# Optimization experiments

Measured on AMD Instinct MI355X. Metric: run time of the kernel, lower is better.

The kernel has to match this reference:

```python
import jax, jax.numpy as jnp
import numpy as np
import math

N_HEAD = 12


def setup_inputs() -> dict:
    key = jax.random.key(0)
    ks = jax.random.split(key, 4)
    B, T, C = 8, 1024, 768
    s = 0.02
    return {
        "x": jax.random.normal(ks[0], (B, T, C), dtype=jnp.float32),
        "attn_mask": jnp.ones((B, T), dtype=jnp.int32),
        "W_attn": jax.random.normal(ks[1], (C, 3 * C), dtype=jnp.float32) * s,
        "b_attn": jnp.zeros((3 * C,), dtype=jnp.float32),
        "W_proj": jax.random.normal(ks[2], (C, C), dtype=jnp.float32) * s,
        "b_proj": jnp.zeros((C,), dtype=jnp.float32),
    }


def reference(x, attn_mask, W_attn, b_attn, W_proj, b_proj):
    B, T, C = x.shape
    hd = C // N_HEAD
    qkv = x @ W_attn + b_attn                      # [B, T, 3C]
    q, k, v = jnp.split(qkv, 3, axis=2)
    # [B, H, T, hd]
    q = q.reshape(B, T, N_HEAD, hd).transpose(0, 2, 1, 3)
    k = k.reshape(B, T, N_HEAD, hd).transpose(0, 2, 1, 3)
    v = v.reshape(B, T, N_HEAD, hd).transpose(0, 2, 1, 3)
    scores = jnp.einsum("bhqd,bhkd->bhqk", q, k) * (1.0 / math.sqrt(hd))
    mask = attn_mask[:, None, None, :]             # [B, 1, 1, T] broadcast over H, q
    scores = jnp.where(mask == 0, -jnp.inf, scores)
    attn = jax.nn.softmax(scores, axis=-1)
    out = jnp.einsum("bhqk,bhkd->bhqd", attn, v)   # [B, H, T, hd]
    out = out.transpose(0, 2, 1, 3).reshape(B, T, C)
    return out @ W_proj + b_proj
```

## Files before the change

### kernel.cpp

```cpp
#include <hip/hip_runtime.h>
#include <hip/hip_bf16.h>
#include <math.h>

constexpr int Bsz  = 8;
constexpr int Tseq = 1024;
constexpr int Cdim = 768;
constexpr int NH   = 12;
constexpr int HD   = 64;
constexpr int Mrows = Bsz * Tseq;
constexpr int C3    = 3 * Cdim;

using short8  = __attribute__((ext_vector_type(8))) short;
using s4v     = __attribute__((ext_vector_type(4))) short;
using floatx4 = __attribute__((ext_vector_type(4))) float;
using uintx4  = __attribute__((ext_vector_type(4))) unsigned int;

__device__ __forceinline__ unsigned short f32_to_bf16_rn(float f) {
    unsigned int u = __float_as_uint(f);
    unsigned int r = u + 0x7FFFu + ((u >> 16) & 1u);
    return (unsigned short)(r >> 16);
}
__device__ __forceinline__ unsigned pack_bf16x2_rn(float a, float b) {
    float2 f2; f2.x = a; f2.y = b;
    __hip_bfloat162 h = __float22bfloat162_rn(f2);
    unsigned r;
    __builtin_memcpy(&r, &h, sizeof(r));
    return r;
}
__device__ __forceinline__ short8 lds_ld8(const unsigned short* p) {
    s4v a = *(const s4v*)p;
    s4v b = *(const s4v*)(p + 4);
    return __builtin_shufflevector(a, b, 0, 1, 2, 3, 4, 5, 6, 7);
}
__device__ __forceinline__ void lds_st8(unsigned short* p, short8 v) {
    *(s4v*)p       = __builtin_shufflevector(v, v, 0, 1, 2, 3);
    *(s4v*)(p + 4) = __builtin_shufflevector(v, v, 4, 5, 6, 7);
}

#define GLOAD_LDS16(g, l) __builtin_amdgcn_global_load_lds(                    \
    (const __attribute__((address_space(1))) void*)(g),                        \
    (__attribute__((address_space(3))) void*)(l), 16, 0, 0)

#define WAITVM0 asm volatile("s_waitcnt vmcnt(0)" ::: "memory")

__global__ __launch_bounds__(256)
void to_bf16(const float* __restrict__ in, unsigned short* __restrict__ out, int n4)
{
    int t = blockIdx.x * blockDim.x + threadIdx.x;
    if (t >= n4) return;
    float4 v = ((const float4*)in)[t];
    ushort4 o;
    o.x = f32_to_bf16_rn(v.x);
    o.y = f32_to_bf16_rn(v.y);
    o.z = f32_to_bf16_rn(v.z);
    o.w = f32_to_bf16_rn(v.w);
    ((ushort4*)out)[t] = o;
}

__global__ __launch_bounds__(256)
void transpose_bf16(const float* __restrict__ in, unsigned short* __restrict__ out,
                    int K, int N)
{
    __shared__ float tile[32][33];
    const int k0 = blockIdx.y * 32, n0 = blockIdx.x * 32;
    const int tx = threadIdx.x & 31, ty = threadIdx.x >> 5;
    #pragma unroll
    for (int r = ty; r < 32; r += 8)
        tile[r][tx] = in[(size_t)(k0 + r) * N + n0 + tx];
    __syncthreads();
    #pragma unroll
    for (int r = ty; r < 32; r += 8)
        out[(size_t)(n0 + r) * K + k0 + tx] = f32_to_bf16_rn(tile[tx][r]);
}

template<bool HM, bool B16>
__device__ __forceinline__ void gemm_body_128x256(
    const unsigned short* __restrict__ A_g,
    const unsigned short* __restrict__ B_g,
    const float* __restrict__ bias,
    void* __restrict__ Cout,
    const int row0, const int col0, const int K, const int N,
    unsigned short* lds)
{
    constexpr int BK   = 32;
    constexpr int ABUF = 4096;
    constexpr int BUFS = 12288;

    const int tid  = threadIdx.x;
    const int wave = tid >> 6;
    const int lane = tid & 63;
    const int lm   = lane & 15;
    const int quad = lane >> 4;
    const int NI   = K / BK;
    const int sq8  = (quad ^ ((lm ^ (lm >> 2)) & 3)) * 8;
    const int sr   = tid >> 2;
    const int sq   = tid & 3;

    floatx4 acc[8][4] = {};

    auto stageA = [&](int buf, int k0) {
        #pragma unroll
        for (int s = 0; s < 2; ++s) {
            const int r  = s * 64 + sr;
            const int gc = ((sq ^ ((r ^ (r >> 2)) & 3)) << 3);
            if constexpr (HM) {
                const int head = k0 >> 6;
                const int off  = (k0 & 63) + gc;
                GLOAD_LDS16(A_g + (size_t)head * (Mrows * HD) +
                            (size_t)(row0 + r) * HD + off,
                            lds + buf * BUFS + r * 32 + sq * 8);
            } else {
                GLOAD_LDS16(A_g + (size_t)(row0 + r) * K + k0 + gc,
                            lds + buf * BUFS + r * 32 + sq * 8);
            }
        }
    };
    auto stageB = [&](int buf, int k0) {
        #pragma unroll
        for (int s = 0; s < 4; ++s) {
            const int r  = s * 64 + sr;
            const int gc = ((sq ^ ((r ^ (r >> 2)) & 3)) << 3);
            GLOAD_LDS16(B_g + (size_t)(col0 + r) * K + k0 + gc,
                        lds + buf * BUFS + ABUF + r * 32 + sq * 8);
        }
    };

    stageA(0, 0);  stageB(0, 0);
    stageA(1, BK); stageB(1, BK);
    asm volatile("s_waitcnt vmcnt(6)" ::: "memory");
    __builtin_amdgcn_s_barrier();

    short8 af[4], bf[4];
    int cur = 0;
    for (int kt = 0; kt < NI; ++kt) {
        const unsigned short* bufA = lds + cur * BUFS;
        const unsigned short* bufB = bufA + ABUF;
        const int  stg  = (cur + 2 >= 3) ? cur - 1 : cur + 2;
        const int  k2   = (kt + 2) * BK;
        const bool doSt = (kt + 2 < NI);

        #pragma unroll
        for (int i = 0; i < 4; ++i)
            af[i] = *(const short8*)(bufA + (i * 16 + lm) * 32 + sq8);
        #pragma unroll
        for (int j = 0; j < 4; ++j)
            bf[j] = *(const short8*)(bufB + (wave * 64 + j * 16 + lm) * 32 + sq8);
        if (doSt) stageA(stg, k2);
        __builtin_amdgcn_s_barrier();
        __builtin_amdgcn_s_setprio(1);
        #pragma unroll
        for (int i = 0; i < 4; ++i)
            #pragma unroll
            for (int j = 0; j < 4; ++j)
                acc[i][j] = __builtin_amdgcn_mfma_f32_16x16x32_bf16(af[i], bf[j], acc[i][j], 0, 0, 0);
        __builtin_amdgcn_s_setprio(0);
        __builtin_amdgcn_s_barrier();

        #pragma unroll
        for (int i = 0; i < 4; ++i)
            af[i] = *(const short8*)(bufA + ((4 + i) * 16 + lm) * 32 + sq8);
        if (doSt) stageB(stg, k2);
        __builtin_amdgcn_s_barrier();
        __builtin_amdgcn_s_setprio(1);
        #pragma unroll
        for (int i = 0; i < 4; ++i)
            #pragma unroll
            for (int j = 0; j < 4; ++j)
                acc[4 + i][j] = __builtin_amdgcn_mfma_f32_16x16x32_bf16(af[i], bf[j], acc[4 + i][j], 0, 0, 0);
        __builtin_amdgcn_s_setprio(0);
        if (kt == NI - 2) { WAITVM0; }
        else if (kt < NI - 2) {
            asm volatile("s_waitcnt vmcnt(6)" ::: "memory");
        }
        __builtin_amdgcn_s_barrier();

        cur = (cur == 2) ? 0 : cur + 1;
    }
    asm volatile("" ::: "memory");

    if constexpr (B16) {
        unsigned short* Cb   = (unsigned short*)Cout;
        unsigned short* wbuf = lds + (NI % 3) * BUFS + wave * 1088;
        float bvj[4];
        #pragma unroll
        for (int j = 0; j < 4; ++j) bvj[j] = bias[col0 + wave * 64 + j * 16 + lm];
        #pragma unroll
        for (int i = 0; i < 8; ++i) {
            #pragma unroll
            for (int j = 0; j < 4; ++j) {
                #pragma unroll
                for (int r = 0; r < 4; ++r)
                    wbuf[(quad * 4 + r) * 68 + j * 16 + lm] = f32_to_bf16_rn(acc[i][j][r] + bvj[j]);
            }
            asm volatile("s_waitcnt lgkmcnt(0)" ::: "memory");
            #pragma unroll
            for (int p = 0; p < 2; ++p) {
                const int lrow  = p * 8 + (lane >> 3);
                const int lcol8 = (lane & 7) * 8;
                short8 v = lds_ld8(&wbuf[lrow * 68 + lcol8]);
                *(short8*)(Cb + (size_t)(row0 + i * 16 + lrow) * N +
                           col0 + wave * 64 + lcol8) = v;
            }
            asm volatile("s_waitcnt lgkmcnt(0)" ::: "memory");
        }
    } else {
        float* C = (float*)Cout;
        #pragma unroll
        for (int j = 0; j < 4; ++j) {
            const int col = col0 + wave * 64 + j * 16 + lm;
            const float bv = bias[col];
            #pragma unroll
            for (int i = 0; i < 8; ++i) {
                const int rowb = row0 + i * 16 + quad * 4;
                #pragma unroll
                for (int r = 0; r < 4; ++r)
                    C[(size_t)(rowb + r) * N + col] = acc[i][j][r] + bv;
            }
        }
    }
}

__global__ __launch_bounds__(256, 2)
void gemm_qkv128(const unsigned short* __restrict__ A_g,
                 const unsigned short* __restrict__ B_g,
                 const float* __restrict__ bias,
                 unsigned short* __restrict__ Cb)
{
    __shared__ __align__(16) unsigned short lds[3 * 12288];
    const int bid = blockIdx.x;
    const int sid = (bid & 7) * 72 + (bid >> 3);
    const int by  = sid & 63;
    const int bx  = sid >> 6;
    gemm_body_128x256<false, true>(A_g, B_g, bias, Cb,
                                   by * 128, bx * 256, Cdim, C3, lds);
}

__global__ __launch_bounds__(256, 3)
void gemm_proj128sq(const unsigned short* __restrict__ AO_g,
                    const unsigned short* __restrict__ B_g,
                    const float* __restrict__ bias,
                    float* __restrict__ C)
{
    constexpr int BK   = 32;
    constexpr int K    = Cdim, N = Cdim;
    constexpr int ABUF = 4096;
    constexpr int BUFS = 8192;
    __shared__ __align__(16) unsigned short lds[3 * BUFS];

    const int tid  = threadIdx.x;
    const int wave = tid >> 6;
    const int lane = tid & 63;
    const int lm   = lane & 15;
    const int quad = lane >> 4;
    const int wy   = wave >> 1, wx = wave & 1;
    const int bid  = blockIdx.x;
    const int sid  = (bid & 7) * 48 + (bid >> 3);
    const int row0 = (sid & 63) * 128;
    const int col0 = (sid >> 6) * 128;
    const int NI   = K / BK;
    const int sq8  = (quad ^ ((lm ^ (lm >> 2)) & 3)) * 8;
    const int sr   = tid >> 2;
    const int sq   = tid & 3;

    floatx4 acc[4][4] = {};

    auto stageA = [&](int buf, int k0) {
        #pragma unroll
        for (int s = 0; s < 2; ++s) {
            const int r  = s * 64 + sr;
            const int gc = ((sq ^ ((r ^ (r >> 2)) & 3)) << 3);
            const int head = k0 >> 6;
            const int off  = (k0 & 63) + gc;
            GLOAD_LDS16(AO_g + (size_t)head * (Mrows * HD) +
                        (size_t)(row0 + r) * HD + off,
                        lds + buf * BUFS + r * 32 + sq * 8);
        }
    };
    auto stageB = [&](int buf, int k0) {
        #pragma unroll
        for (int s = 0; s < 2; ++s) {
            const int r  = s * 64 + sr;
            const int gc = ((sq ^ ((r ^ (r >> 2)) & 3)) << 3);
            GLOAD_LDS16(B_g + (size_t)(col0 + r) * K + k0 + gc,
                        lds + buf * BUFS + ABUF + r * 32 + sq * 8);
        }
    };

    stageA(0, 0);  stageB(0, 0);
    stageA(1, BK); stageB(1, BK);
    asm volatile("s_waitcnt vmcnt(4)" ::: "memory");
    __builtin_amdgcn_s_barrier();

    short8 af[4], bf[4];
    int cur = 0;
    for (int kt = 0; kt < NI; ++kt) {
        const unsigned short* bufA = lds + cur * BUFS;
        const unsigned short* bufB = bufA + ABUF;
        const int  stg  = (cur + 2 >= 3) ? cur - 1 : cur + 2;
        const int  k2   = (kt + 2) * BK;
        const bool doSt = (kt + 2 < NI);

        #pragma unroll
        for (int i = 0; i < 4; ++i)
            af[i] = *(const short8*)(bufA + (wy * 64 + i * 16 + lm) * 32 + sq8);
        #pragma unroll
        for (int j = 0; j < 2; ++j)
            bf[j] = *(const short8*)(bufB + (wx * 64 + j * 16 + lm) * 32 + sq8);
        if (doSt) stageA(stg, k2);
        __builtin_amdgcn_s_barrier();
        __builtin_amdgcn_s_setprio(1);
        #pragma unroll
        for (int i = 0; i < 4; ++i)
            #pragma unroll
            for (int j = 0; j < 2; ++j)
                acc[i][j] = __builtin_amdgcn_mfma_f32_16x16x32_bf16(af[i], bf[j], acc[i][j], 0, 0, 0);
        __builtin_amdgcn_s_setprio(0);
        __builtin_amdgcn_s_barrier();

        #pragma unroll
        for (int j = 2; j < 4; ++j)
            bf[j] = *(const short8*)(bufB + (wx * 64 + j * 16 + lm) * 32 + sq8);
        if (doSt) stageB(stg, k2);
        __builtin_amdgcn_s_barrier();
        __builtin_amdgcn_s_setprio(1);
        #pragma unroll
        for (int i = 0; i < 4; ++i)
            #pragma unroll
            for (int j = 2; j < 4; ++j)
                acc[i][j] = __builtin_amdgcn_mfma_f32_16x16x32_bf16(af[i], bf[j], acc[i][j], 0, 0, 0);
        __builtin_amdgcn_s_setprio(0);
        if (kt == NI - 2) { WAITVM0; }
        else if (kt < NI - 2) {
            asm volatile("s_waitcnt vmcnt(4)" ::: "memory");
        }
        __builtin_amdgcn_s_barrier();

        cur = (cur == 2) ? 0 : cur + 1;
    }
    asm volatile("" ::: "memory");

    #pragma unroll
    for (int j = 0; j < 4; ++j) {
        const int col = col0 + wx * 64 + j * 16 + lm;
        const float bv = bias[col];
        #pragma unroll
        for (int i = 0; i < 4; ++i) {
            const int rowb = row0 + wy * 64 + i * 16 + quad * 4;
            #pragma unroll
            for (int r = 0; r < 4; ++r)
                C[(size_t)(rowb + r) * N + col] = acc[i][j][r] + bv;
        }
    }
}

__global__ __launch_bounds__(256, 3)
void attn_bf16(const unsigned short* __restrict__ qkv,
               const int* __restrict__ mask,
               unsigned short* __restrict__ outh)
{
    constexpr int LDW = 68;
    constexpr int NT  = Tseq / 64;
    __shared__ __align__(16) unsigned short Kh[2][64 * LDW];
    __shared__ __align__(16) unsigned short Vh[2][64 * LDW];
    __shared__ float maskadd[2][64];
    __shared__ int   mflag[2];

    const int tid  = threadIdx.x;
    const int wave = tid >> 6;
    const int lane = tid & 63;
    const int lm   = lane & 15;
    const int quad = lane >> 4;
    const int idx  = blockIdx.x;
    const int bh   = idx % (Bsz * NH);
    const int qb   = idx / (Bsz * NH);
    const int b    = bh / NH;
    const int h    = bh % NH;
    const int q0   = qb * 128;
    const float scale = 0.125f;

    short8 qf[2][2];
    #pragma unroll
    for (int mt = 0; mt < 2; ++mt) {
        const size_t qrow = (size_t)(b * Tseq + q0 + wave * 32 + mt * 16 + lm) * C3 + h * HD;
        #pragma unroll
        for (int kf = 0; kf < 2; ++kf)
            qf[mt][kf] = *(const short8*)(qkv + qrow + kf * 32 + quad * 8);
    }

    const int tr0 = (tid & 31) * 2;
    const int sc  = (tid >> 5) * 8;
    const int ps0 = (tr0 & 0x27) | ((tr0 & 0x10) >> 1) | ((tr0 & 0x08) << 1);
    const int smi = (tid & 0x27) | ((tid & 0x10) >> 1) | ((tid & 0x08) << 1);

    short8 kh0, kh1, vh0, vh1;
    float  mreg = 0.f;

    {
        const size_t g0 = (size_t)(b * Tseq + tr0) * C3 + Cdim + h * HD + sc;
        kh0 = *(const short8*)(qkv + g0);
        kh1 = *(const short8*)(qkv + g0 + C3);
        vh0 = *(const short8*)(qkv + g0 + Cdim);
        vh1 = *(const short8*)(qkv + g0 + Cdim + C3);
        lds_st8(&Kh[0][ps0 * LDW + sc], kh0);
        lds_st8(&Kh[0][(ps0 + 1) * LDW + sc], kh1);
        #pragma unroll
        for (int i = 0; i < 8; ++i) {
            unsigned int pv = (unsigned int)(unsigned short)vh0[i] |
                              ((unsigned int)(unsigned short)vh1[i] << 16);
            *(unsigned int*)&Vh[0][(sc + i) * LDW + tr0] = pv;
        }
        if (tid < 64) {
            mreg = (mask[b * Tseq + tid] == 0) ? -1e30f : 0.0f;
            const int f = __all(mreg == 0.0f);
            maskadd[0][smi] = mreg;
            if (tid == 0) mflag[0] = f;
        }
    }
    __syncthreads();

    floatx4 O[2][4] = {};
    float lsum[2] = {0.f, 0.f};

    for (int kt = 0; kt < NT; ++kt) {
        const int cur = kt & 1;
        const int nxt = cur ^ 1;
        const unsigned short* Khc = Kh[cur];
        const unsigned short* Vhc = Vh[cur];

        if (kt + 1 < NT) {
            const size_t g0 = (size_t)(b * Tseq + (kt + 1) * 64 + tr0) * C3 + Cdim + h * HD + sc;
            kh0 = *(const short8*)(qkv + g0);
            kh1 = *(const short8*)(qkv + g0 + C3);
            vh0 = *(const short8*)(qkv + g0 + Cdim);
            vh1 = *(const short8*)(qkv + g0 + Cdim + C3);
            if (tid < 64) mreg = (mask[b * Tseq + (kt + 1) * 64 + tid] == 0) ? -1e30f : 0.0f;
        }

        floatx4 S[2][4] = {};
        #pragma unroll
        for (int kf = 0; kf < 2; ++kf) {
            short8 kh[4];
            #pragma unroll
            for (int nt = 0; nt < 4; ++nt)
                kh[nt] = lds_ld8(&Khc[(nt * 16 + lm) * LDW + kf * 32 + quad * 8]);
            #pragma unroll
            for (int mt = 0; mt < 2; ++mt)
                #pragma unroll
                for (int nt = 0; nt < 4; ++nt)
                    S[mt][nt] = __builtin_amdgcn_mfma_f32_16x16x32_bf16(kh[nt], qf[mt][kf], S[mt][nt], 0, 0, 0);
        }

        const int nomask = mflag[cur];

        unsigned X[2][8];
        if (nomask) {
            #pragma unroll
            for (int mt = 0; mt < 2; ++mt) {
                #pragma unroll
                for (int nt = 0; nt < 4; ++nt) {
                    float p0 = __expf(S[mt][nt][0] * scale);
                    float p1 = __expf(S[mt][nt][1] * scale);
                    float p2 = __expf(S[mt][nt][2] * scale);
                    float p3 = __expf(S[mt][nt][3] * scale);
                    lsum[mt] += p0; lsum[mt] += p1;
                    lsum[mt] += p2; lsum[mt] += p3;
                    X[mt][nt * 2 + 0] = pack_bf16x2_rn(p0, p1);
                    X[mt][nt * 2 + 1] = pack_bf16x2_rn(p2, p3);
                }
            }
        } else {
            float madd[4][4];
            #pragma unroll
            for (int nt = 0; nt < 4; ++nt)
                #pragma unroll
                for (int r = 0; r < 4; ++r)
                    madd[nt][r] = maskadd[cur][nt * 16 + quad * 4 + r];
            #pragma unroll
            for (int mt = 0; mt < 2; ++mt) {
                #pragma unroll
                for (int nt = 0; nt < 4; ++nt) {
                    float p0 = __expf(S[mt][nt][0] * scale + madd[nt][0]);
                    float p1 = __expf(S[mt][nt][1] * scale + madd[nt][1]);
                    float p2 = __expf(S[mt][nt][2] * scale + madd[nt][2]);
                    float p3 = __expf(S[mt][nt][3] * scale + madd[nt][3]);
                    lsum[mt] += p0; lsum[mt] += p1;
                    lsum[mt] += p2; lsum[mt] += p3;
                    X[mt][nt * 2 + 0] = pack_bf16x2_rn(p0, p1);
                    X[mt][nt * 2 + 1] = pack_bf16x2_rn(p2, p3);
                }
            }
        }

        const bool qodd = (quad & 1);
        short8 pf[2][2];
        #pragma unroll
        for (int mt = 0; mt < 2; ++mt) {
            #pragma unroll
            for (int pr = 0; pr < 4; ++pr) {
                const int a  = (pr & 1) | ((pr & 2) << 1);
                const int b2 = a + 2;
                unsigned t = qodd ? X[mt][a] : X[mt][b2];
                t = (unsigned)__shfl_xor((int)t, 16);
                X[mt][a]  = qodd ? t : X[mt][a];
                X[mt][b2] = qodd ? X[mt][b2] : t;
            }
            uintx4 u0 = {X[mt][0], X[mt][1], X[mt][2], X[mt][3]};
            uintx4 u1 = {X[mt][4], X[mt][5], X[mt][6], X[mt][7]};
            __builtin_memcpy(&pf[mt][0], &u0, 16);
            __builtin_memcpy(&pf[mt][1], &u1, 16);
        }

        #pragma unroll
        for (int kf = 0; kf < 2; ++kf) {
            #pragma unroll
            for (int dt = 0; dt < 4; ++dt) {
                short8 vh = lds_ld8(&Vhc[(dt * 16 + lm) * LDW + kf * 32 + quad * 8]);
                #pragma unroll
                for (int mt = 0; mt < 2; ++mt)
                    O[mt][dt] = __builtin_amdgcn_mfma_f32_16x16x32_bf16(vh, pf[mt][kf], O[mt][dt], 0, 0, 0);
            }
        }

        if (kt + 1 < NT) {
            lds_st8(&Kh[nxt][ps0 * LDW + sc], kh0);
            lds_st8(&Kh[nxt][(ps0 + 1) * LDW + sc], kh1);
            #pragma unroll
            for (int i = 0; i < 8; ++i) {
                unsigned int pv = (unsigned int)(unsigned short)vh0[i] |
                                  ((unsigned int)(unsigned short)vh1[i] << 16);
                *(unsigned int*)&Vh[nxt][(sc + i) * LDW + tr0] = pv;
            }
            if (tid < 64) {
                const int f = __all(mreg == 0.0f);
                maskadd[nxt][smi] = mreg;
                if (tid == 0) mflag[nxt] = f;
            }
        }
        __syncthreads();
    }

    #pragma unroll
    for (int mt = 0; mt < 2; ++mt) {
        lsum[mt] += __shfl_xor(lsum[mt], 16);
        lsum[mt] += __shfl_xor(lsum[mt], 32);
        const float inv_l = 1.0f / lsum[mt];
        const size_t row = (size_t)h * (Mrows * HD) +
                           (size_t)(b * Tseq + q0 + wave * 32 + mt * 16 + lm) * HD;
        #pragma unroll
        for (int dt = 0; dt < 4; ++dt) {
            ushort4 hv;
            unsigned short* hp = &hv.x;
            #pragma unroll
            for (int r = 0; r < 4; ++r)
                hp[r] = f32_to_bf16_rn(O[mt][dt][r] * inv_l);
            *(ushort4*)(outh + row + dt * 16 + quad * 4) = hv;
        }
    }
}

extern "C" void kernel_launch(void* const* d_in, const int* in_sizes, int n_in,
                              void* d_out, int out_size, void* d_ws, size_t ws_size,
                              hipStream_t stream)
{
    const float* x      = (const float*)d_in[0];
    const int*   mask   = (const int*)  d_in[1];
    const float* W_attn = (const float*)d_in[2];
    const float* b_attn = (const float*)d_in[3];
    const float* W_proj = (const float*)d_in[4];
    const float* b_proj = (const float*)d_in[5];
    float* out = (float*)d_out;

    unsigned short* xh    = (unsigned short*)d_ws;
    unsigned short* wat_h = xh    + (size_t)Mrows * Cdim;
    unsigned short* wpt_h = wat_h + (size_t)C3 * Cdim;
    unsigned short* qkvh  = wpt_h + (size_t)Cdim * Cdim;
    unsigned short* aoh   = xh;

    dim3 blk(256);

    to_bf16<<<dim3(Mrows * Cdim / 4 / 256), blk, 0, stream>>>(x, xh, Mrows * Cdim / 4);
    transpose_bf16<<<dim3(C3 / 32, Cdim / 32), blk, 0, stream>>>(W_attn, wat_h, Cdim, C3);
    transpose_bf16<<<dim3(Cdim / 32, Cdim / 32), blk, 0, stream>>>(W_proj, wpt_h, Cdim, Cdim);

    gemm_qkv128<<<dim3(576), blk, 0, stream>>>(xh, wat_h, b_attn, qkvh);

    attn_bf16<<<dim3((Tseq / 128) * Bsz * NH), blk, 0, stream>>>(qkvh, mask, aoh);

    gemm_proj128sq<<<dim3(384), blk, 0, stream>>>(aoh, wpt_h, b_proj, out);
}
```

Before: 205.0 us.

## Fuse prep kernels, drop intra-iteration GEMM barriers, split softmax sum accumulators

Merges the bf16 conversion of x and the two weight transposes into one launch keyed on block index. Removes three of the four s_barriers per k-iteration in both GEMM main loops, relying on the triple-buffer distance for safety. In attention, replaces per-iteration address recomputation with incremented pointers and splits the row-sum into two accumulators to shorten the dependency chain. Dropping the barriers risks LDS read/write races between waves.

```diff
diff --git a/kernel.cpp b/kernel.cpp
--- a/kernel.cpp
+++ b/kernel.cpp
@@ -44,25 +44,35 @@
 #define WAITVM0 asm volatile("s_waitcnt vmcnt(0)" ::: "memory")
 
 __global__ __launch_bounds__(256)
-void to_bf16(const float* __restrict__ in, unsigned short* __restrict__ out, int n4)
-{
-    int t = blockIdx.x * blockDim.x + threadIdx.x;
-    if (t >= n4) return;
-    float4 v = ((const float4*)in)[t];
-    ushort4 o;
-    o.x = f32_to_bf16_rn(v.x);
-    o.y = f32_to_bf16_rn(v.y);
-    o.z = f32_to_bf16_rn(v.z);
-    o.w = f32_to_bf16_rn(v.w);
-    ((ushort4*)out)[t] = o;
-}
-
-__global__ __launch_bounds__(256)
-void transpose_bf16(const float* __restrict__ in, unsigned short* __restrict__ out,
-                    int K, int N)
+void prep_all(const float* __restrict__ x,      unsigned short* __restrict__ xh,
+              const float* __restrict__ W_attn, unsigned short* __restrict__ wat_h,
+              const float* __restrict__ W_proj, unsigned short* __restrict__ wpt_h)
 {
     __shared__ float tile[32][33];
-    const int k0 = blockIdx.y * 32, n0 = blockIdx.x * 32;
+    const int bid = blockIdx.x;
+    if (bid < 6144) {
+        const int t = bid * 256 + threadIdx.x;
+        float4 v = ((const float4*)x)[t];
+        ushort4 o;
+        o.x = f32_to_bf16_rn(v.x);
+        o.y = f32_to_bf16_rn(v.y);
+        o.z = f32_to_bf16_rn(v.z);
+        o.w = f32_to_bf16_rn(v.w);
+        ((ushort4*)xh)[t] = o;
+        return;
+    }
+    const float* in; unsigned short* out; int N, bx, by;
+    if (bid < 6144 + 1728) {
+        const int r = bid - 6144;
+        in = W_attn; out = wat_h; N = C3;
+        bx = r % 72; by = r / 72;
+    } else {
+        const int r = bid - 7872;
+        in = W_proj; out = wpt_h; N = Cdim;
+        bx = r % 24; by = r / 24;
+    }
+    const int K  = Cdim;
+    const int k0 = by * 32, n0 = bx * 32;
     const int tx = threadIdx.x & 31, ty = threadIdx.x >> 5;
     #pragma unroll
     for (int r = ty; r < 32; r += 8)
@@ -146,7 +156,6 @@
         for (int j = 0; j < 4; ++j)
             bf[j] = *(const short8*)(bufB + (wave * 64 + j * 16 + lm) * 32 + sq8);
         if (doSt) stageA(stg, k2);
-        __builtin_amdgcn_s_barrier();
         __builtin_amdgcn_s_setprio(1);
         #pragma unroll
         for (int i = 0; i < 4; ++i)
@@ -154,13 +163,11 @@
             for (int j = 0; j < 4; ++j)
                 acc[i][j] = __builtin_amdgcn_mfma_f32_16x16x32_bf16(af[i], bf[j], acc[i][j], 0, 0, 0);
         __builtin_amdgcn_s_setprio(0);
-        __builtin_amdgcn_s_barrier();
 
         #pragma unroll
         for (int i = 0; i < 4; ++i)
             af[i] = *(const short8*)(bufA + ((4 + i) * 16 + lm) * 32 + sq8);
         if (doSt) stageB(stg, k2);
-        __builtin_amdgcn_s_barrier();
         __builtin_amdgcn_s_setprio(1);
         #pragma unroll
         for (int i = 0; i < 4; ++i)
@@ -168,6 +175,7 @@
             for (int j = 0; j < 4; ++j)
                 acc[4 + i][j] = __builtin_amdgcn_mfma_f32_16x16x32_bf16(af[i], bf[j], acc[4 + i][j], 0, 0, 0);
         __builtin_amdgcn_s_setprio(0);
+
         if (kt == NI - 2) { WAITVM0; }
         else if (kt < NI - 2) {
             asm volatile("s_waitcnt vmcnt(6)" ::: "memory");
@@ -307,7 +315,6 @@
         for (int j = 0; j < 2; ++j)
             bf[j] = *(const short8*)(bufB + (wx * 64 + j * 16 + lm) * 32 + sq8);
         if (doSt) stageA(stg, k2);
-        __builtin_amdgcn_s_barrier();
         __builtin_amdgcn_s_setprio(1);
         #pragma unroll
         for (int i = 0; i < 4; ++i)
@@ -315,13 +322,11 @@
             for (int j = 0; j < 2; ++j)
                 acc[i][j] = __builtin_amdgcn_mfma_f32_16x16x32_bf16(af[i], bf[j], acc[i][j], 0, 0, 0);
         __builtin_amdgcn_s_setprio(0);
-        __builtin_amdgcn_s_barrier();
 
         #pragma unroll
         for (int j = 2; j < 4; ++j)
             bf[j] = *(const short8*)(bufB + (wx * 64 + j * 16 + lm) * 32 + sq8);
         if (doSt) stageB(stg, k2);
-        __builtin_amdgcn_s_barrier();
         __builtin_amdgcn_s_setprio(1);
         #pragma unroll
         for (int i = 0; i < 4; ++i)
@@ -329,6 +334,7 @@
             for (int j = 2; j < 4; ++j)
                 acc[i][j] = __builtin_amdgcn_mfma_f32_16x16x32_bf16(af[i], bf[j], acc[i][j], 0, 0, 0);
         __builtin_amdgcn_s_setprio(0);
+
         if (kt == NI - 2) { WAITVM0; }
         else if (kt < NI - 2) {
             asm volatile("s_waitcnt vmcnt(4)" ::: "memory");
@@ -395,12 +401,14 @@
     short8 kh0, kh1, vh0, vh1;
     float  mreg = 0.f;
 
+    size_t gcur = (size_t)(b * Tseq + tr0) * C3 + Cdim + h * HD + sc;
+    int    mcur = b * Tseq + tid;
+
     {
-        const size_t g0 = (size_t)(b * Tseq + tr0) * C3 + Cdim + h * HD + sc;
-        kh0 = *(const short8*)(qkv + g0);
-        kh1 = *(const short8*)(qkv + g0 + C3);
-        vh0 = *(const short8*)(qkv + g0 + Cdim);
-        vh1 = *(const short8*)(qkv + g0 + Cdim + C3);
+        kh0 = *(const short8*)(qkv + gcur);
+        kh1 = *(const short8*)(qkv + gcur + C3);
+        vh0 = *(const short8*)(qkv + gcur + Cdim);
+        vh1 = *(const short8*)(qkv + gcur + Cdim + C3);
         lds_st8(&Kh[0][ps0 * LDW + sc], kh0);
         lds_st8(&Kh[0][(ps0 + 1) * LDW + sc], kh1);
         #pragma unroll
@@ -410,7 +418,7 @@
             *(unsigned int*)&Vh[0][(sc + i) * LDW + tr0] = pv;
         }
         if (tid < 64) {
-            mreg = (mask[b * Tseq + tid] == 0) ? -1e30f : 0.0f;
+            mreg = (mask[mcur] == 0) ? -1e30f : 0.0f;
             const int f = __all(mreg == 0.0f);
             maskadd[0][smi] = mreg;
             if (tid == 0) mflag[0] = f;
@@ -419,7 +427,8 @@
     __syncthreads();
 
     floatx4 O[2][4] = {};
-    float lsum[2] = {0.f, 0.f};
+    float lsA[2] = {0.f, 0.f};
+    float lsB[2] = {0.f, 0.f};
 
     for (int kt = 0; kt < NT; ++kt) {
         const int cur = kt & 1;
@@ -428,12 +437,13 @@
         const unsigned short* Vhc = Vh[cur];
 
         if (kt + 1 < NT) {
-            const size_t g0 = (size_t)(b * Tseq + (kt + 1) * 64 + tr0) * C3 + Cdim + h * HD + sc;
-            kh0 = *(const short8*)(qkv + g0);
-            kh1 = *(const short8*)(qkv + g0 + C3);
-            vh0 = *(const short8*)(qkv + g0 + Cdim);
-            vh1 = *(const short8*)(qkv + g0 + Cdim + C3);
-            if (tid < 64) mreg = (mask[b * Tseq + (kt + 1) * 64 + tid] == 0) ? -1e30f : 0.0f;
+            gcur += (size_t)64 * C3;
+            mcur += 64;
+            kh0 = *(const short8*)(qkv + gcur);
+            kh1 = *(const short8*)(qkv + gcur + C3);
+            vh0 = *(const short8*)(qkv + gcur + Cdim);
+            vh1 = *(const short8*)(qkv + gcur + Cdim + C3);
+            if (tid < 64) mreg = (mask[mcur] == 0) ? -1e30f : 0.0f;
         }
 
         floatx4 S[2][4] = {};
@@ -462,8 +472,8 @@
                     float p1 = __expf(S[mt][nt][1] * scale);
                     float p2 = __expf(S[mt][nt][2] * scale);
                     float p3 = __expf(S[mt][nt][3] * scale);
-                    lsum[mt] += p0; lsum[mt] += p1;
-                    lsum[mt] += p2; lsum[mt] += p3;
+                    lsA[mt] += p0; lsB[mt] += p1;
+                    lsA[mt] += p2; lsB[mt] += p3;
                     X[mt][nt * 2 + 0] = pack_bf16x2_rn(p0, p1);
                     X[mt][nt * 2 + 1] = pack_bf16x2_rn(p2, p3);
                 }
@@ -483,8 +493,8 @@
                     float p1 = __expf(S[mt][nt][1] * scale + madd[nt][1]);
                     float p2 = __expf(S[mt][nt][2] * scale + madd[nt][2]);
                     float p3 = __expf(S[mt][nt][3] * scale + madd[nt][3]);
-                    lsum[mt] += p0; lsum[mt] += p1;
-                    lsum[mt] += p2; lsum[mt] += p3;
+                    lsA[mt] += p0; lsB[mt] += p1;
+                    lsA[mt] += p2; lsB[mt] += p3;
                     X[mt][nt * 2 + 0] = pack_bf16x2_rn(p0, p1);
                     X[mt][nt * 2 + 1] = pack_bf16x2_rn(p2, p3);
                 }
@@ -541,9 +551,10 @@
 
     #pragma unroll
     for (int mt = 0; mt < 2; ++mt) {
-        lsum[mt] += __shfl_xor(lsum[mt], 16);
-        lsum[mt] += __shfl_xor(lsum[mt], 32);
-        const float inv_l = 1.0f / lsum[mt];
+        float lsum = lsA[mt] + lsB[mt];
+        lsum += __shfl_xor(lsum, 16);
+        lsum += __shfl_xor(lsum, 32);
+        const float inv_l = 1.0f / lsum;
         const size_t row = (size_t)h * (Mrows * HD) +
                            (size_t)(b * Tseq + q0 + wave * 32 + mt * 16 + lm) * HD;
         #pragma unroll
@@ -578,9 +589,7 @@
 
     dim3 blk(256);
 
-    to_bf16<<<dim3(Mrows * Cdim / 4 / 256), blk, 0, stream>>>(x, xh, Mrows * Cdim / 4);
-    transpose_bf16<<<dim3(C3 / 32, Cdim / 32), blk, 0, stream>>>(W_attn, wat_h, Cdim, C3);
-    transpose_bf16<<<dim3(Cdim / 32, Cdim / 32), blk, 0, stream>>>(W_proj, wpt_h, Cdim, Cdim);
+    prep_all<<<dim3(8448), blk, 0, stream>>>(x, xh, W_attn, wat_h, W_proj, wpt_h);
 
     gemm_qkv128<<<dim3(576), blk, 0, stream>>>(xh, wat_h, b_attn, qkvh);
 
```

New measurement: 200.7 us. -2.1%, faster.
